# Performance work log

Measured on AMD Instinct MI355X. Metric: run time of the kernel, lower is better.

Reference implementation:

```python
import jax, jax.numpy as jnp
import numpy as np

B, T, I, H = 4096, 128, 32, 64


def _u(key, shape, bound):
    return jax.random.uniform(key, shape, jnp.float32, -bound, bound)


def setup_inputs() -> dict:
    key = jax.random.key(0)
    ks = jax.random.split(key, 14)
    bound = 1.0 / np.sqrt(H)  # torch LSTM/Linear default init scale
    inp = {
        "x": jax.random.normal(ks[0], (B, T, I), jnp.float32),
        "Wih0": _u(ks[1], (4 * H, I), bound),
        "Whh0": _u(ks[2], (4 * H, H), bound),
        "bih0": _u(ks[3], (4 * H,), bound),
        "bhh0": _u(ks[4], (4 * H,), bound),
        "Wih1": _u(ks[5], (4 * H, H), bound),
        "Whh1": _u(ks[6], (4 * H, H), bound),
        "bih1": _u(ks[7], (4 * H,), bound),
        "bhh1": _u(ks[8], (4 * H,), bound),
        "Wc1": _u(ks[9], (32, H), 1.0 / np.sqrt(H)),
        "bc1": _u(ks[10], (32,), 1.0 / np.sqrt(H)),
        "Wc2": _u(ks[11], (1, 32), 1.0 / np.sqrt(32)),
        "bc2": _u(ks[12], (1,), 1.0 / np.sqrt(32)),
    }
    return inp


def lstm_layer(x_tbi, Wih, Whh, bih, bhh):
    """x_tbi: [T, B, in]. Returns (all hidden [T,B,H], final hidden [B,H]).
    PyTorch gate order: i, f, g, o."""
    b = x_tbi.shape[1]
    h0 = jnp.zeros((b, Whh.shape[1]), x_tbi.dtype)
    c0 = jnp.zeros_like(h0)
    # precompute input projections for all timesteps in one big GEMM
    xproj = jnp.einsum('tbi,gi->tbg', x_tbi, Wih) + (bih + bhh)

    def step(carry, xp_t):
        h, c = carry
        gates = xp_t + h @ Whh.T  # [B, 4H]
        i, f, g, o = jnp.split(gates, 4, axis=-1)
        c = jax.nn.sigmoid(f) * c + jax.nn.sigmoid(i) * jnp.tanh(g)
        h = jax.nn.sigmoid(o) * jnp.tanh(c)
        return (h, c), h

    (hT, _), hs = jax.lax.scan(step, (h0, c0), xproj)
    return hs, hT


def reference(x, Wih0, Whh0, bih0, bhh0, Wih1, Whh1, bih1, bhh1, Wc1, bc1, Wc2, bc2):
    x_tbi = jnp.transpose(x, (1, 0, 2))  # [T, B, I]
    hs0, _ = lstm_layer(x_tbi, Wih0, Whh0, bih0, bhh0)
    # dropout between layers is identity in eval mode
    _, hT = lstm_layer(hs0, Wih1, Whh1, bih1, bhh1)  # h_n[-1]: [B, H]
    hidden = jax.nn.relu(hT @ Wc1.T + bc1)  # [B, 32]; classifier dropout = identity (eval)
    out = hidden @ Wc2.T + bc2  # [B, 1]
    return out.squeeze(-1)  # [B]
```

## Files before the change

kernel.cpp:

```cpp
#include <hip/hip_runtime.h>


#define TT 128
#define II 32

typedef _Float16 half8 __attribute__((ext_vector_type(8)));
typedef float floatx4 __attribute__((ext_vector_type(4)));

#define LOG2E 1.4426950408889634f

__device__ __forceinline__ half8 cvt_frag(float4 a, float4 b) {
    half8 h;
    h[0] = (_Float16)a.x; h[1] = (_Float16)a.y; h[2] = (_Float16)a.z; h[3] = (_Float16)a.w;
    h[4] = (_Float16)b.x; h[5] = (_Float16)b.y; h[6] = (_Float16)b.z; h[7] = (_Float16)b.w;
    return h;
}

__device__ __forceinline__ half8 load_w_frag(const float* __restrict__ W, int n, int K, int k0) {
    const float* p = W + (size_t)n * K + k0;
    return cvt_frag(*(const float4*)p, *(const float4*)(p + 4));
}

__device__ __forceinline__ void lstm_cell4(const floatx4* a, float* cr, float* hnew,
                                           float nbi, float nbf, float bg2, float nbo) {
    const float nL  = -LOG2E;
    const float p2L = 2.0f * LOG2E;
    const float C43 = 30.0f * LOG2E;
    float m[4], numc[4];
    #pragma unroll
    for (int r = 0; r < 4; ++r) {
        float vf = __builtin_amdgcn_exp2f(fmaf(a[1][r], nL, nbf));
        float tg = __builtin_amdgcn_fmed3f(fmaf(a[2][r], p2L, bg2), -C43, C43);
        float u  = __builtin_amdgcn_exp2f(tg);
        float vi = __builtin_amdgcn_exp2f(fmaf(a[0][r], nL, nbi));
        float du = u + 1.0f;
        float ds = fmaf(vi, du, du);
        float df = 1.0f + vf;
        m[r]    = df * ds;
        numc[r] = fmaf(cr[r], ds, (u - 1.0f) * df);
    }
    float p01 = m[0] * m[1], p23 = m[2] * m[3];
    float r01 = __builtin_amdgcn_rcpf(p01);
    float r23 = __builtin_amdgcn_rcpf(p23);
    float c0 = numc[0] * (r01 * m[1]);
    float c1 = numc[1] * (r01 * m[0]);
    float c2 = numc[2] * (r23 * m[3]);
    float c3 = numc[3] * (r23 * m[2]);
    float c[4] = {c0, c1, c2, c3};
    float dh[4], un[4];
    #pragma unroll
    for (int r = 0; r < 4; ++r) {
        cr[r] = c[r];
        float vo = __builtin_amdgcn_exp2f(fmaf(a[3][r], nL, nbo));
        float tc = __builtin_amdgcn_fmed3f(c[r] * p2L, -C43, C43);
        float uc = __builtin_amdgcn_exp2f(tc);
        float du2 = uc + 1.0f;
        dh[r] = fmaf(vo, du2, du2);
        un[r] = uc - 1.0f;
    }
    float q01 = dh[0] * dh[1], q23 = dh[2] * dh[3];
    float s01 = __builtin_amdgcn_rcpf(q01);
    float s23 = __builtin_amdgcn_rcpf(q23);
    hnew[0] = un[0] * (s01 * dh[1]);
    hnew[1] = un[1] * (s01 * dh[0]);
    hnew[2] = un[2] * (s23 * dh[3]);
    hnew[3] = un[3] * (s23 * dh[2]);
}

__global__ __launch_bounds__(512, 2) void lstm_fused(
    const float* __restrict__ x,
    const float* __restrict__ Wih0, const float* __restrict__ Whh0,
    const float* __restrict__ bih0, const float* __restrict__ bhh0,
    const float* __restrict__ Wih1, const float* __restrict__ Whh1,
    const float* __restrict__ bih1, const float* __restrict__ bhh1,
    const float* __restrict__ Wc1, const float* __restrict__ bc1,
    const float* __restrict__ Wc2, const float* __restrict__ bc2,
    float* __restrict__ out)
{
    __shared__ __align__(16) _Float16 xs[2][16][40];
    __shared__ __align__(16) _Float16 h0s[2][16][72];
    __shared__ __align__(16) _Float16 h1s[2][16][72];
    __shared__ __align__(16) float h1f[16][68];
    __shared__ float hid[16][32];

    const int tid  = threadIdx.x;
    const int wid  = tid >> 6;
    const int w4   = wid & 3;
    const bool isL0 = (wid < 4);
    const int lane = tid & 63;
    const int q  = lane >> 4;
    const int lr = lane & 15;
    const int b0 = blockIdx.x * 16;

    const float nL  = -LOG2E;
    const float p2L = 2.0f * LOG2E;

    half8 bx0[4], bh0[4][2];
    half8 bi1[4][2], bh1[4][2];
    float bias[4];
    if (isL0) {
        #pragma unroll
        for (int g = 0; g < 4; ++g) {
            int n = (w4 + 4 * g) * 16 + lr;
            bx0[g]    = load_w_frag(Wih0, n, 32, q * 8);
            bh0[g][0] = load_w_frag(Whh0, n, 64, q * 8);
            bh0[g][1] = load_w_frag(Whh0, n, 64, 32 + q * 8);
            bias[g]   = bih0[n] + bhh0[n];
        }
    } else {
        #pragma unroll
        for (int g = 0; g < 4; ++g) {
            int n = (w4 + 4 * g) * 16 + lr;
            bi1[g][0] = load_w_frag(Wih1, n, 64, q * 8);
            bi1[g][1] = load_w_frag(Wih1, n, 64, 32 + q * 8);
            bh1[g][0] = load_w_frag(Whh1, n, 64, q * 8);
            bh1[g][1] = load_w_frag(Whh1, n, 64, 32 + q * 8);
            bias[g]   = bih1[n] + bhh1[n];
        }
    }
    const float nbi = nL * bias[0], nbf = nL * bias[1];
    const float bg2 = p2L * bias[2], nbo = nL * bias[3];
    const floatx4 zeroq = {0.f, 0.f, 0.f, 0.f};

    for (int i = tid; i < 2 * 16 * 72; i += 512) {
        ((_Float16*)h0s)[i] = (_Float16)0.0f;
        ((_Float16*)h1s)[i] = (_Float16)0.0f;
    }

    const int xm = (tid >> 4) & 15;
    const int xf = (tid & 15) * 2;
    const float* xrow = x + ((size_t)(b0 + xm) * TT) * II + xf;
    float2 xbuf = {0.f, 0.f};
    if (isL0) {
        float2 x0 = *(const float2*)(xrow);
        xs[0][xm][xf]     = (_Float16)x0.x;
        xs[0][xm][xf + 1] = (_Float16)x0.y;
        xbuf = *(const float2*)(xrow + II);
    }

    float cr[4] = {0.f, 0.f, 0.f, 0.f};
    float hnew[4];
    floatx4 a0[4];
    floatx4 a1[4];

    for (int k = 0; k < TT + 2; ++k) {
        __syncthreads();
        const bool l0k = isL0 && (k < TT);
        float2 xnew = xbuf;
        if (l0k) {
            half8 xfrag = *(const half8*)&xs[k & 1][lr][q * 8];
            half8 h0a   = *(const half8*)&h0s[(k + 1) & 1][lr][q * 8];
            half8 h0b   = *(const half8*)&h0s[(k + 1) & 1][lr][32 + q * 8];
            if (k + 2 < TT) xnew = *(const float2*)(xrow + (size_t)(k + 2) * II);
            #pragma unroll
            for (int g = 0; g < 4; ++g) {
                floatx4 acc = __builtin_amdgcn_mfma_f32_16x16x32_f16(xfrag, bx0[g],    zeroq, 0, 0, 0);
                acc         = __builtin_amdgcn_mfma_f32_16x16x32_f16(h0a,   bh0[g][0], acc,   0, 0, 0);
                a0[g]       = __builtin_amdgcn_mfma_f32_16x16x32_f16(h0b,   bh0[g][1], acc,   0, 0, 0);
            }
        }
        if (!isL0 && k >= 2) {
            lstm_cell4(a1, cr, hnew, nbi, nbf, bg2, nbo);
            if (k - 2 == TT - 1) {
                #pragma unroll
                for (int r = 0; r < 4; ++r)
                    h1f[q * 4 + r][w4 * 16 + lr] = hnew[r];
            } else {
                #pragma unroll
                for (int r = 0; r < 4; ++r)
                    h1s[k & 1][q * 4 + r][w4 * 16 + lr] = (_Float16)hnew[r];
            }
        }

        __syncthreads();
        if (l0k) {
            lstm_cell4(a0, cr, hnew, nbi, nbf, bg2, nbo);
            #pragma unroll
            for (int r = 0; r < 4; ++r)
                h0s[k & 1][q * 4 + r][w4 * 16 + lr] = (_Float16)hnew[r];
            if (k + 1 < TT) {
                xs[(k + 1) & 1][xm][xf]     = (_Float16)xbuf.x;
                xs[(k + 1) & 1][xm][xf + 1] = (_Float16)xbuf.y;
            }
            xbuf = xnew;
        }
        if (!isL0 && k >= 1 && k <= TT) {
            half8 g0a = *(const half8*)&h0s[(k - 1) & 1][lr][q * 8];
            half8 g0b = *(const half8*)&h0s[(k - 1) & 1][lr][32 + q * 8];
            half8 h1a = *(const half8*)&h1s[k & 1][lr][q * 8];
            half8 h1b = *(const half8*)&h1s[k & 1][lr][32 + q * 8];
            #pragma unroll
            for (int g = 0; g < 4; ++g) {
                floatx4 acc = __builtin_amdgcn_mfma_f32_16x16x32_f16(g0a, bi1[g][0], zeroq, 0, 0, 0);
                acc         = __builtin_amdgcn_mfma_f32_16x16x32_f16(g0b, bi1[g][1], acc,   0, 0, 0);
                acc         = __builtin_amdgcn_mfma_f32_16x16x32_f16(h1a, bh1[g][0], acc,   0, 0, 0);
                a1[g]       = __builtin_amdgcn_mfma_f32_16x16x32_f16(h1b, bh1[g][1], acc,   0, 0, 0);
            }
        }
    }
    __syncthreads();

    if (tid < 256) {
        int m = tid >> 4;
        int u = (tid & 15) * 2;
        float aa = bc1[u], bb = bc1[u + 1];
        const float* w0 = Wc1 + u * 64;
        const float* w1 = Wc1 + (u + 1) * 64;
        #pragma unroll 8
        for (int kk = 0; kk < 64; ++kk) {
            float hv = h1f[m][kk];
            aa += hv * w0[kk];
            bb += hv * w1[kk];
        }
        hid[m][u]     = fmaxf(aa, 0.f);
        hid[m][u + 1] = fmaxf(bb, 0.f);
    }
    __syncthreads();
    if (tid < 16) {
        float o = bc2[0];
        #pragma unroll
        for (int u = 0; u < 32; ++u) o += hid[tid][u] * Wc2[u];
        out[b0 + tid] = o;
    }
}

extern "C" void kernel_launch(void* const* d_in, const int* in_sizes, int n_in,
                              void* d_out, int out_size, void* d_ws, size_t ws_size,
                              hipStream_t stream) {
    (void)in_sizes; (void)n_in; (void)d_ws; (void)ws_size; (void)out_size;
    const float* x    = (const float*)d_in[0];
    const float* Wih0 = (const float*)d_in[1];
    const float* Whh0 = (const float*)d_in[2];
    const float* bih0 = (const float*)d_in[3];
    const float* bhh0 = (const float*)d_in[4];
    const float* Wih1 = (const float*)d_in[5];
    const float* Whh1 = (const float*)d_in[6];
    const float* bih1 = (const float*)d_in[7];
    const float* bhh1 = (const float*)d_in[8];
    const float* Wc1  = (const float*)d_in[9];
    const float* bc1  = (const float*)d_in[10];
    const float* Wc2  = (const float*)d_in[11];
    const float* bc2  = (const float*)d_in[12];
    lstm_fused<<<dim3(256), dim3(512), 0, stream>>>(
        x, Wih0, Whh0, bih0, bhh0, Wih1, Whh1, bih1, bhh1, Wc1, bc1, Wc2, bc2,
        (float*)d_out);
}
```

Measured before the change: 227.9 us.

## Collapse two-barrier wavefront schedule into a single barrier per step

Restructures the layer-0/layer-1 wavefront loop so each iteration has one __syncthreads instead of two. Each layer's warps now run their MFMA gate GEMM and cell update back to back before writing hidden state into double-buffered shared memory. The previous schedule split GEMM and cell across two barrier phases. This removes one block-wide barrier per timestep and shortens the loop by one iteration, but puts GEMM and activation in series inside each warp, which may reduce overlap between the two layers' warp groups.

```diff
diff --git a/kernel.cpp b/kernel.cpp
--- a/kernel.cpp
+++ b/kernel.cpp
@@ -39,14 +39,13 @@
         m[r]    = df * ds;
         numc[r] = fmaf(cr[r], ds, (u - 1.0f) * df);
     }
-    float p01 = m[0] * m[1], p23 = m[2] * m[3];
-    float r01 = __builtin_amdgcn_rcpf(p01);
-    float r23 = __builtin_amdgcn_rcpf(p23);
-    float c0 = numc[0] * (r01 * m[1]);
-    float c1 = numc[1] * (r01 * m[0]);
-    float c2 = numc[2] * (r23 * m[3]);
-    float c3 = numc[3] * (r23 * m[2]);
-    float c[4] = {c0, c1, c2, c3};
+    float r01 = __builtin_amdgcn_rcpf(m[0] * m[1]);
+    float r23 = __builtin_amdgcn_rcpf(m[2] * m[3]);
+    float c[4];
+    c[0] = numc[0] * (r01 * m[1]);
+    c[1] = numc[1] * (r01 * m[0]);
+    c[2] = numc[2] * (r23 * m[3]);
+    c[3] = numc[3] * (r23 * m[2]);
     float dh[4], un[4];
     #pragma unroll
     for (int r = 0; r < 4; ++r) {
@@ -58,9 +57,8 @@
         dh[r] = fmaf(vo, du2, du2);
         un[r] = uc - 1.0f;
     }
-    float q01 = dh[0] * dh[1], q23 = dh[2] * dh[3];
-    float s01 = __builtin_amdgcn_rcpf(q01);
-    float s23 = __builtin_amdgcn_rcpf(q23);
+    float s01 = __builtin_amdgcn_rcpf(dh[0] * dh[1]);
+    float s23 = __builtin_amdgcn_rcpf(dh[2] * dh[3]);
     hnew[0] = un[0] * (s01 * dh[1]);
     hnew[1] = un[1] * (s01 * dh[0]);
     hnew[2] = un[2] * (s23 * dh[3]);
@@ -135,66 +133,69 @@
         float2 x0 = *(const float2*)(xrow);
         xs[0][xm][xf]     = (_Float16)x0.x;
         xs[0][xm][xf + 1] = (_Float16)x0.y;
-        xbuf = *(const float2*)(xrow + II);
+        if (TT > 1) xbuf = *(const float2*)(xrow + 1 * II);
     }
 
     float cr[4] = {0.f, 0.f, 0.f, 0.f};
-    float hnew[4];
-    floatx4 a0[4];
-    floatx4 a1[4];
-
-    for (int k = 0; k < TT + 2; ++k) {
+
+    for (int k = 0; k <= TT; ++k) {
         __syncthreads();
-        const bool l0k = isL0 && (k < TT);
+
+        const int rd = (k + 1) & 1;
+        const int wr = k & 1;
+        const bool doL0 = isL0 && (k < TT);
+        const bool doL1 = (!isL0) && (k >= 1);
+        floatx4 a[4];
+        float hnew[4];
         float2 xnew = xbuf;
-        if (l0k) {
-            half8 xfrag = *(const half8*)&xs[k & 1][lr][q * 8];
-            half8 h0a   = *(const half8*)&h0s[(k + 1) & 1][lr][q * 8];
-            half8 h0b   = *(const half8*)&h0s[(k + 1) & 1][lr][32 + q * 8];
+
+        if (doL0) {
+            half8 xfrag = *(const half8*)&xs[wr][lr][q * 8];
+            half8 h0a   = *(const half8*)&h0s[rd][lr][q * 8];
+            half8 h0b   = *(const half8*)&h0s[rd][lr][32 + q * 8];
             if (k + 2 < TT) xnew = *(const float2*)(xrow + (size_t)(k + 2) * II);
             #pragma unroll
             for (int g = 0; g < 4; ++g) {
                 floatx4 acc = __builtin_amdgcn_mfma_f32_16x16x32_f16(xfrag, bx0[g],    zeroq, 0, 0, 0);
                 acc         = __builtin_amdgcn_mfma_f32_16x16x32_f16(h0a,   bh0[g][0], acc,   0, 0, 0);
-                a0[g]       = __builtin_amdgcn_mfma_f32_16x16x32_f16(h0b,   bh0[g][1], acc,   0, 0, 0);
-            }
-        }
-        if (!isL0 && k >= 2) {
-            lstm_cell4(a1, cr, hnew, nbi, nbf, bg2, nbo);
-            if (k - 2 == TT - 1) {
+                a[g]        = __builtin_amdgcn_mfma_f32_16x16x32_f16(h0b,   bh0[g][1], acc,   0, 0, 0);
+            }
+            lstm_cell4(a, cr, hnew, nbi, nbf, bg2, nbo);
+        }
+        if (doL1) {
+            half8 g0a = *(const half8*)&h0s[rd][lr][q * 8];
+            half8 g0b = *(const half8*)&h0s[rd][lr][32 + q * 8];
+            half8 h1a = *(const half8*)&h1s[rd][lr][q * 8];
+            half8 h1b = *(const half8*)&h1s[rd][lr][32 + q * 8];
+            #pragma unroll
+            for (int g = 0; g < 4; ++g) {
+                floatx4 acc = __builtin_amdgcn_mfma_f32_16x16x32_f16(g0a, bi1[g][0], zeroq, 0, 0, 0);
+                acc         = __builtin_amdgcn_mfma_f32_16x16x32_f16(g0b, bi1[g][1], acc,   0, 0, 0);
+                acc         = __builtin_amdgcn_mfma_f32_16x16x32_f16(h1a, bh1[g][0], acc,   0, 0, 0);
+                a[g]        = __builtin_amdgcn_mfma_f32_16x16x32_f16(h1b, bh1[g][1], acc,   0, 0, 0);
+            }
+            lstm_cell4(a, cr, hnew, nbi, nbf, bg2, nbo);
+        }
+
+        if (doL0) {
+            #pragma unroll
+            for (int r = 0; r < 4; ++r)
+                h0s[wr][q * 4 + r][w4 * 16 + lr] = (_Float16)hnew[r];
+            if (k + 1 < TT) {
+                xs[rd][xm][xf]     = (_Float16)xbuf.x;
+                xs[rd][xm][xf + 1] = (_Float16)xbuf.y;
+            }
+            xbuf = xnew;
+        }
+        if (doL1) {
+            if (k == TT) {
                 #pragma unroll
                 for (int r = 0; r < 4; ++r)
                     h1f[q * 4 + r][w4 * 16 + lr] = hnew[r];
             } else {
                 #pragma unroll
                 for (int r = 0; r < 4; ++r)
-                    h1s[k & 1][q * 4 + r][w4 * 16 + lr] = (_Float16)hnew[r];
-            }
-        }
-
-        __syncthreads();
-        if (l0k) {
-            lstm_cell4(a0, cr, hnew, nbi, nbf, bg2, nbo);
-            #pragma unroll
-            for (int r = 0; r < 4; ++r)
-                h0s[k & 1][q * 4 + r][w4 * 16 + lr] = (_Float16)hnew[r];
-            if (k + 1 < TT) {
-                xs[(k + 1) & 1][xm][xf]     = (_Float16)xbuf.x;
-                xs[(k + 1) & 1][xm][xf + 1] = (_Float16)xbuf.y;
-            }
-            xbuf = xnew;
-        }
-        if (!isL0 && k >= 1 && k <= TT) {
-            half8 g0a = *(const half8*)&h0s[(k - 1) & 1][lr][q * 8];
-            half8 g0b = *(const half8*)&h0s[(k - 1) & 1][lr][32 + q * 8];
-            half8 h1a = *(const half8*)&h1s[k & 1][lr][q * 8];
-            half8 h1b = *(const half8*)&h1s[k & 1][lr][32 + q * 8];
-            #pragma unroll
-            for (int g = 0; g < 4; ++g) {
-                floatx4 acc = __builtin_amdgcn_mfma_f32_16x16x32_f16(g0a, bi1[g][0], zeroq, 0, 0, 0);
-                acc         = __builtin_amdgcn_mfma_f32_16x16x32_f16(g0b, bi1[g][1], acc,   0, 0, 0);
-                acc         = __builtin_amdgcn_mfma_f32_16x16x32_f16(h1a, bh1[g][0], acc,   0, 0, 0);
-                a1[g]       = __builtin_amdgcn_mfma_f32_16x16x32_f16(h1b, bh1[g][1], acc,   0, 0, 0);
+                    h1s[wr][q * 4 + r][w4 * 16 + lr] = (_Float16)hnew[r];
             }
         }
     }
```

After: 202.9 us. 11.0% less time.
